# Kernel optimization log

Measured on AMD Instinct MI355X. Metric: run time of the kernel, lower is better.

Reference implementation:

```python
import jax, jax.numpy as jnp
import numpy as np

N_HEAD = 16

def _alibi_slopes(num_heads):
    # m_i = (256 ** (1/num_heads)) ** -(i+1)
    x = (2.0 ** 8) ** (1.0 / num_heads)
    return jnp.asarray([1.0 / x ** (i + 1) for i in range(num_heads)], dtype=jnp.float32)

def setup_inputs() -> dict:
    key = jax.random.key(0)
    k1, k2 = jax.random.split(key)
    B, S, D = 2, 2048, 1024
    x = jax.random.normal(k1, (B, S, D), dtype=jnp.float32)
    W_kqv = jax.random.normal(k2, (D, 3 * D), dtype=jnp.float32) * 0.02
    return {"x": x, "W_kqv": W_kqv}

def reference(x, W_kqv):
    B, S, D = x.shape
    H = N_HEAD
    hd = D // H
    scale = jnp.sqrt(jnp.asarray(D, dtype=x.dtype))  # NOTE: sqrt(n_embd), per source
    kqv = x @ W_kqv                                   # [B,S,3D]
    k, q, v = jnp.split(kqv, 3, axis=-1)              # chunk order: key, query, value
    q = q.reshape(B, S, H, hd).transpose(0, 2, 1, 3)  # [B,H,S,hd]
    k = k.reshape(B, S, H, hd).transpose(0, 2, 1, 3)
    v = v.reshape(B, S, H, hd).transpose(0, 2, 1, 3)
    # ALiBi bias: m[h] * (j - i)
    pos = jnp.arange(S)
    rel = (pos[None, :] - pos[:, None]).astype(x.dtype)      # [S,S]
    m = _alibi_slopes(H).astype(x.dtype)                     # [H]
    bias = m[:, None, None] * rel                            # [H,S,S]
    score = jnp.einsum('bhqd,bhkd->bhqk', q, k) / scale + bias[None]
    causal = pos[None, :] <= pos[:, None]                    # [S,S] lower-tri
    score = jnp.where(causal[None, None], score, -jnp.inf)
    attn = jax.nn.softmax(score, axis=-1)                    # [B,H,S,S]
    out = jnp.einsum('bhqk,bhkd->bhqd', attn, v)
    out = out.transpose(0, 2, 1, 3).reshape(B, S, D)
    return (out, attn)
```

## Files before the change

### kernel.cpp

```cpp
#include <hip/hip_runtime.h>
#include <hip/hip_bf16.h>

typedef __attribute__((ext_vector_type(8))) short short8;
typedef __attribute__((ext_vector_type(4))) float f32x4;

static __device__ __forceinline__ unsigned short f2bf(float f) {
    unsigned int x = __float_as_uint(f);
    x += 0x7fffu + ((x >> 16) & 1u);
    return (unsigned short)(x >> 16);
}

static __device__ __forceinline__ void gld_lds16(const unsigned short* g, unsigned short* l) {
    __builtin_amdgcn_global_load_lds((const __attribute__((address_space(1))) void*)g,
                                     (__attribute__((address_space(3))) void*)l, 16, 0, 0);
}

__global__ __launch_bounds__(256) void cvt_x_kernel(const float* __restrict__ in,
                                                    unsigned short* __restrict__ outb,
                                                    int n4) {
    int i = blockIdx.x * 256 + threadIdx.x;
    if (i < n4) {
        f32x4 v = *(const f32x4*)(in + (size_t)i * 4);
        ushort4 o;
        o.x = f2bf(v[0]); o.y = f2bf(v[1]); o.z = f2bf(v[2]); o.w = f2bf(v[3]);
        *(ushort4*)(outb + (size_t)i * 4) = o;
    }
}

__global__ __launch_bounds__(256) void cvt_wt_kernel(const float* __restrict__ W,
                                                     unsigned short* __restrict__ WT) {
    __shared__ float t[64][65];
    const int n0 = blockIdx.x * 64;
    const int k0 = blockIdx.y * 64;
    const int tid = threadIdx.x;
#pragma unroll
    for (int i = 0; i < 16; ++i) {
        int lin = tid + i * 256;
        int rr = lin >> 6, cc = lin & 63;
        t[rr][cc] = W[(size_t)(k0 + rr) * 3072 + n0 + cc];
    }
    __syncthreads();
#pragma unroll
    for (int i = 0; i < 16; ++i) {
        int lin = tid + i * 256;
        int nn = lin >> 6, kk = lin & 63;
        WT[(size_t)(n0 + nn) * 1024 + k0 + kk] = f2bf(t[kk][nn]);
    }
}

__global__ __launch_bounds__(256) void gemm_kqv_kernel(
    const unsigned short* __restrict__ A,
    const unsigned short* __restrict__ BT,
    unsigned short* __restrict__ qb,
    unsigned short* __restrict__ kb,
    unsigned short* __restrict__ vtb) {
    __shared__ __attribute__((aligned(16))) unsigned short smem[2 * 128 * 72];
    unsigned short (*As)[64] = (unsigned short(*)[64])smem;
    unsigned short (*Bs)[64] = (unsigned short(*)[64])(smem + 128 * 64);
    const int tid = threadIdx.x;
    const int w = tid >> 6, lane = tid & 63;
    const int quad = lane >> 4, cl = lane & 15;

    const int wg = (int)blockIdx.x + 24 * (int)blockIdx.y;
    const int wgs = (wg & 7) * 96 + (wg >> 3);
    const int m0 = (wgs / 24) * 128, n0 = (wgs % 24) * 128;
    const int wm = (w >> 1) * 64, wn = (w & 1) * 64;

    const int srow = lane >> 3;
    const int schk = (lane & 7) ^ srow;
    const unsigned short* Ap = A + (size_t)(m0 + w * 32 + srow) * 1024 + schk * 8;
    const unsigned short* Bp = BT + (size_t)(n0 + w * 32 + srow) * 1024 + schk * 8;

    f32x4 acc[4][4] = {};

    for (int kk = 0; kk < 1024; kk += 64) {
#pragma unroll
        for (int i = 0; i < 4; ++i) {
            gld_lds16(Ap + kk + (size_t)i * 8 * 1024, &As[w * 32 + i * 8][0]);
            gld_lds16(Bp + kk + (size_t)i * 8 * 1024, &Bs[w * 32 + i * 8][0]);
        }
        __syncthreads();
#pragma unroll
        for (int kc = 0; kc < 2; ++kc) {
            short8 af[4], bfr[4];
#pragma unroll
            for (int i = 0; i < 4; ++i) {
                const int col = ((kc * 4 + quad) ^ (cl & 7)) * 8;
                af[i] = *(const short8*)&As[wm + i * 16 + cl][col];
                bfr[i] = *(const short8*)&Bs[wn + i * 16 + cl][col];
            }
#pragma unroll
            for (int im = 0; im < 4; ++im)
#pragma unroll
                for (int in = 0; in < 4; ++in)
                    acc[im][in] = __builtin_amdgcn_mfma_f32_16x16x32_bf16(
                        af[im], bfr[in], acc[im][in], 0, 0, 0);
        }
        __syncthreads();
    }
    unsigned short (*Cs)[130] = (unsigned short(*)[130])smem;

    const int chunk = n0 >> 10;
    const int d0 = n0 & 1023;
    const int b = m0 >> 11;
    const int s_base = m0 & 2047;

    if (chunk == 2) {
#pragma unroll
        for (int im = 0; im < 4; ++im)
#pragma unroll
            for (int in = 0; in < 4; ++in)
#pragma unroll
                for (int rg = 0; rg < 4; ++rg)
                    Cs[wn + in * 16 + cl][wm + im * 16 + quad * 4 + rg] =
                        f2bf(acc[im][in][rg]);
        __syncthreads();
#pragma unroll
        for (int it = 0; it < 8; ++it) {
            int l = it * 2048 + tid * 8;
            int c = l >> 7;
            int r = l & 127;
            int d = d0 + c, hh = d >> 6, dd = d & 63;
            size_t dst = ((size_t)(b * 16 + hh) * 64 + dd) * 2048 + s_base + r;
            *(uint4*)(vtb + dst) = *(const uint4*)&Cs[c][r];
        }
    } else {
#pragma unroll
        for (int im = 0; im < 4; ++im)
#pragma unroll
            for (int in = 0; in < 4; ++in)
#pragma unroll
                for (int rg = 0; rg < 4; ++rg)
                    Cs[wm + im * 16 + quad * 4 + rg][wn + in * 16 + cl] =
                        f2bf(acc[im][in][rg]);
        __syncthreads();
        unsigned short* outp = (chunk == 0) ? kb : qb;
#pragma unroll
        for (int it = 0; it < 8; ++it) {
            int l = it * 2048 + tid * 8;
            int r = l >> 7;
            int c = l & 127;
            int d = d0 + c, hh = d >> 6, dd = d & 63;
            size_t dst = ((size_t)(b * 16 + hh) * 2048 + s_base + r) * 64 + dd;
            *(uint4*)(outp + dst) = *(const uint4*)&Cs[r][c];
        }
    }
}

__global__ __launch_bounds__(256, 2) void attn_kernel(
    const unsigned short* __restrict__ qb,
    const unsigned short* __restrict__ kb,
    const unsigned short* __restrict__ vtb,
    float* __restrict__ out_,
    float* __restrict__ attn) {
    const int h = blockIdx.y;
    const int b = blockIdx.z;
    const int bh = b * 16 + h;
    const int tid = threadIdx.x;
    const int w = tid >> 6;
    const int lane = tid & 63;
    const int quad = lane >> 4;
    const int cl = lane & 15;

    const unsigned short* Qh = qb + (size_t)bh * 2048 * 64;
    const unsigned short* Kh = kb + (size_t)bh * 2048 * 64;
    const unsigned short* Vh = vtb + (size_t)bh * 64 * 2048;
    float* attnh = attn + (size_t)bh * 2048 * 2048;

    __shared__ __attribute__((aligned(16))) unsigned short Kt[2][64][64];
    __shared__ __attribute__((aligned(16))) unsigned short Vt[2][64][64];
    __shared__ __attribute__((aligned(16))) unsigned short Ps[4][16][64];

    const int srow = lane >> 3;
    const int schk = (lane & 7) ^ srow;

    auto stageK = [&](int jt, int buf) {
#pragma unroll
        for (int i = 0; i < 2; ++i)
            gld_lds16(Kh + (size_t)(jt * 64 + w * 16 + i * 8 + srow) * 64 + schk * 8,
                      &Kt[buf][w * 16 + i * 8][0]);
    };
    auto stageV = [&](int j0, int buf) {
#pragma unroll
        for (int i = 0; i < 2; ++i)
            gld_lds16(Vh + (size_t)(w * 16 + i * 8 + srow) * 2048 + j0 + schk * 8,
                      &Vt[buf][w * 16 + i * 8][0]);
    };

    const float mh = exp2f(-0.5f * (float)(h + 1));
    const float sc1 = 1.0f / 32.0f;

    for (int half = 0; half < 2; ++half) {
        const int t64 = half ? 31 - (int)blockIdx.x : (int)blockIdx.x;
        const int q0 = t64 * 64;
        const int row0 = q0 + w * 16;
        const int jtmax = t64;

        short8 aq0 = *(const short8*)(Qh + (size_t)(row0 + cl) * 64 + quad * 8);
        short8 aq1 = *(const short8*)(Qh + (size_t)(row0 + cl) * 64 + 32 + quad * 8);

        float rsum[4] = {0.f, 0.f, 0.f, 0.f};
        __syncthreads();
        stageK(0, 0);
        {
            int cur = 0;
            for (int jt = 0; jt <= jtmax; ++jt, cur ^= 1) {
                __syncthreads();
                if (jt < jtmax) stageK(jt + 1, cur ^ 1);
                const int j0 = jt * 64;
#pragma unroll
                for (int nt = 0; nt < 4; ++nt) {
                    const int r = nt * 16 + cl;
                    short8 k0 = *(const short8*)&Kt[cur][r][((quad) ^ (cl & 7)) * 8];
                    short8 k1 = *(const short8*)&Kt[cur][r][((quad + 4) ^ (cl & 7)) * 8];
                    f32x4 s = {0.f, 0.f, 0.f, 0.f};
                    s = __builtin_amdgcn_mfma_f32_16x16x32_bf16(aq0, k0, s, 0, 0, 0);
                    s = __builtin_amdgcn_mfma_f32_16x16x32_bf16(aq1, k1, s, 0, 0, 0);
                    const int jc = j0 + nt * 16 + cl;
#pragma unroll
                    for (int rg = 0; rg < 4; ++rg) {
                        int irow = row0 + quad * 4 + rg;
                        if (jc <= irow)
                            rsum[rg] += __expf(s[rg] * sc1 + mh * (float)(jc - irow));
                    }
                }
            }
        }
#pragma unroll
        for (int rg = 0; rg < 4; ++rg) {
            float v = rsum[rg];
            v += __shfl_xor(v, 1);
            v += __shfl_xor(v, 2);
            v += __shfl_xor(v, 4);
            v += __shfl_xor(v, 8);
            rsum[rg] = 1.0f / v;
        }

        __syncthreads();
        f32x4 oacc[4] = {};
        stageK(0, 0);
        stageV(0, 0);
        {
            int cur = 0;
            for (int jt = 0; jt <= jtmax; ++jt, cur ^= 1) {
                __syncthreads();
                if (jt < jtmax) {
                    stageK(jt + 1, cur ^ 1);
                    stageV(jt * 64 + 64, cur ^ 1);
                }
                const int j0 = jt * 64;
                f32x4 sv[4];
#pragma unroll
                for (int nt = 0; nt < 4; ++nt) {
                    const int r = nt * 16 + cl;
                    short8 k0 = *(const short8*)&Kt[cur][r][((quad) ^ (cl & 7)) * 8];
                    short8 k1 = *(const short8*)&Kt[cur][r][((quad + 4) ^ (cl & 7)) * 8];
                    f32x4 s = {0.f, 0.f, 0.f, 0.f};
                    s = __builtin_amdgcn_mfma_f32_16x16x32_bf16(aq0, k0, s, 0, 0, 0);
                    sv[nt] = __builtin_amdgcn_mfma_f32_16x16x32_bf16(aq1, k1, s, 0, 0, 0);
                }
#pragma unroll
                for (int nt = 0; nt < 4; ++nt) {
                    const int jc = j0 + nt * 16 + cl;
#pragma unroll
                    for (int rg = 0; rg < 4; ++rg) {
                        const int irow = row0 + quad * 4 + rg;
                        float p = (jc <= irow)
                                      ? __expf(sv[nt][rg] * sc1 + mh * (float)(jc - irow)) * rsum[rg]
                                      : 0.f;
                        Ps[w][quad * 4 + rg]
                          [(((nt * 2 + (cl >> 3)) ^ ((quad * 4 + rg) & 7)) << 3) | (cl & 7)] =
                            f2bf(p);
                        __builtin_nontemporal_store(p, attnh + (size_t)irow * 2048 + jc);
                    }
                }

                short8 pa0 = *(const short8*)&Ps[w][cl][((quad ^ (cl & 7)) << 3)];
                short8 pa1 = *(const short8*)&Ps[w][cl][((((quad + 4)) ^ (cl & 7)) << 3)];

#pragma unroll
                for (int on = 0; on < 4; ++on) {
                    const int r = on * 16 + cl;
                    short8 v0 = *(const short8*)&Vt[cur][r][((quad) ^ (cl & 7)) * 8];
                    short8 v1 = *(const short8*)&Vt[cur][r][((quad + 4) ^ (cl & 7)) * 8];
                    oacc[on] = __builtin_amdgcn_mfma_f32_16x16x32_bf16(pa0, v0, oacc[on], 0, 0, 0);
                    oacc[on] = __builtin_amdgcn_mfma_f32_16x16x32_bf16(pa1, v1, oacc[on], 0, 0, 0);
                }
            }
        }

#pragma unroll
        for (int on = 0; on < 4; ++on) {
#pragma unroll
            for (int rg = 0; rg < 4; ++rg) {
                int srow2 = row0 + quad * 4 + rg;
                __builtin_nontemporal_store(
                    oacc[on][rg], out_ + ((size_t)b * 2048 + srow2) * 1024 + h * 64 + on * 16 + cl);
            }
        }

        const int jz = (jtmax + 1) * 64;
        if (jz < 2048) {
            f32x4 z = {0.f, 0.f, 0.f, 0.f};
            for (int rr = 0; rr < 16; ++rr) {
                float* dst = attnh + (size_t)(row0 + rr) * 2048;
                for (int c = jz + lane * 4; c < 2048; c += 256)
                    __builtin_nontemporal_store(z, (f32x4*)(dst + c));
            }
        }
    }
}

extern "C" void kernel_launch(void* const* d_in, const int* in_sizes, int n_in,
                              void* d_out, int out_size, void* d_ws, size_t ws_size,
                              hipStream_t stream) {
    const float* x = (const float*)d_in[0];
    const float* Wk = (const float*)d_in[1];
    float* out = (float*)d_out;
    float* attn = out + (size_t)2 * 2048 * 1024;

    unsigned short* xb = (unsigned short*)d_ws;
    unsigned short* wtb = xb + (size_t)4096 * 1024;
    unsigned short* qb = wtb + (size_t)3072 * 1024;
    unsigned short* kb = qb + (size_t)32 * 2048 * 64;
    unsigned short* vtb = kb + (size_t)32 * 2048 * 64;

    cvt_x_kernel<<<dim3(4096), dim3(256), 0, stream>>>(x, xb, 4096 * 1024 / 4);
    cvt_wt_kernel<<<dim3(48, 16), dim3(256), 0, stream>>>(Wk, wtb);
    gemm_kqv_kernel<<<dim3(24, 32), dim3(256), 0, stream>>>(xb, wtb, qb, kb, vtb);
    attn_kernel<<<dim3(16, 16, 2), dim3(256), 0, stream>>>(qb, kb, vtb, out, attn);
}
```

Before: 692.4 us.

## Restructure QKV GEMM to 256x256 tiles with double-buffered LDS prefetch

The projection GEMM moves from 128x128 tiles with 4 waves to 256x256 tiles with 8 waves. It double-buffers the LDS tiles so the next K-slice is loaded while MFMAs run, and raises wave priority around the MFMA blocks. The V-transpose epilogue gets an XOR-swizzled LDS staging layout, and the K/Q epilogue now writes scalar bf16 stores directly instead of staging through LDS. The grid shrinks to 192 blocks on a 256-CU part, so fewer CUs are busy, and the direct scalar stores may be less coalesced.

After: 687.0 us. Within noise of the previous version (-0.8%).

```diff
diff --git a/kernel.cpp b/kernel.cpp
--- a/kernel.cpp
+++ b/kernel.cpp
@@ -48,57 +48,83 @@
     }
 }
 
-__global__ __launch_bounds__(256) void gemm_kqv_kernel(
+__global__ __launch_bounds__(512, 2) void gemm_kqv_kernel(
     const unsigned short* __restrict__ A,
     const unsigned short* __restrict__ BT,
     unsigned short* __restrict__ qb,
     unsigned short* __restrict__ kb,
     unsigned short* __restrict__ vtb) {
-    __shared__ __attribute__((aligned(16))) unsigned short smem[2 * 128 * 72];
-    unsigned short (*As)[64] = (unsigned short(*)[64])smem;
-    unsigned short (*Bs)[64] = (unsigned short(*)[64])(smem + 128 * 64);
+    __shared__ __attribute__((aligned(16))) unsigned short smem[2 * 2 * 256 * 64];
+    unsigned short (*As)[256][64] = (unsigned short(*)[256][64])smem;
+    unsigned short (*Bs)[256][64] = (unsigned short(*)[256][64])(smem + 2 * 256 * 64);
     const int tid = threadIdx.x;
     const int w = tid >> 6, lane = tid & 63;
     const int quad = lane >> 4, cl = lane & 15;
 
-    const int wg = (int)blockIdx.x + 24 * (int)blockIdx.y;
-    const int wgs = (wg & 7) * 96 + (wg >> 3);
-    const int m0 = (wgs / 24) * 128, n0 = (wgs % 24) * 128;
-    const int wm = (w >> 1) * 64, wn = (w & 1) * 64;
+    const int wg = (int)blockIdx.x + 12 * (int)blockIdx.y;
+    const int wgs = (wg & 7) * 24 + (wg >> 3);
+    const int m0 = (wgs / 12) * 256, n0 = (wgs % 12) * 256;
+    const int wm = (w >> 2) * 128, wn = (w & 3) * 64;
 
     const int srow = lane >> 3;
     const int schk = (lane & 7) ^ srow;
-    const unsigned short* Ap = A + (size_t)(m0 + w * 32 + srow) * 1024 + schk * 8;
-    const unsigned short* Bp = BT + (size_t)(n0 + w * 32 + srow) * 1024 + schk * 8;
-
-    f32x4 acc[4][4] = {};
-
-    for (int kk = 0; kk < 1024; kk += 64) {
-#pragma unroll
-        for (int i = 0; i < 4; ++i) {
-            gld_lds16(Ap + kk + (size_t)i * 8 * 1024, &As[w * 32 + i * 8][0]);
-            gld_lds16(Bp + kk + (size_t)i * 8 * 1024, &Bs[w * 32 + i * 8][0]);
-        }
-        __syncthreads();
-#pragma unroll
-        for (int kc = 0; kc < 2; ++kc) {
-            short8 af[4], bfr[4];
-#pragma unroll
-            for (int i = 0; i < 4; ++i) {
-                const int col = ((kc * 4 + quad) ^ (cl & 7)) * 8;
-                af[i] = *(const short8*)&As[wm + i * 16 + cl][col];
-                bfr[i] = *(const short8*)&Bs[wn + i * 16 + cl][col];
-            }
-#pragma unroll
-            for (int im = 0; im < 4; ++im)
-#pragma unroll
-                for (int in = 0; in < 4; ++in)
-                    acc[im][in] = __builtin_amdgcn_mfma_f32_16x16x32_bf16(
-                        af[im], bfr[in], acc[im][in], 0, 0, 0);
-        }
-        __syncthreads();
-    }
-    unsigned short (*Cs)[130] = (unsigned short(*)[130])smem;
+    const unsigned short* Ap = A + (size_t)(m0 + w * 8 + srow) * 1024 + schk * 8;
+    const unsigned short* Bp = BT + (size_t)(n0 + w * 8 + srow) * 1024 + schk * 8;
+
+    f32x4 acc[8][4] = {};
+
+    auto stageA = [&](int kk, int buf) {
+#pragma unroll
+        for (int i = 0; i < 4; ++i)
+            gld_lds16(Ap + kk + (size_t)i * 64 * 1024, &As[buf][i * 64 + w * 8][0]);
+    };
+    auto stageB = [&](int kk, int buf) {
+#pragma unroll
+        for (int i = 0; i < 4; ++i)
+            gld_lds16(Bp + kk + (size_t)i * 64 * 1024, &Bs[buf][i * 64 + w * 8][0]);
+    };
+
+    stageA(0, 0);
+    stageB(0, 0);
+
+    for (int kt = 0; kt < 16; ++kt) {
+        const int cur = kt & 1;
+        asm volatile("s_waitcnt vmcnt(0)" ::: "memory");
+        __builtin_amdgcn_s_barrier();
+
+        short8 bfr[4][2];
+#pragma unroll
+        for (int n = 0; n < 4; ++n)
+#pragma unroll
+            for (int kc = 0; kc < 2; ++kc)
+                bfr[n][kc] = *(const short8*)
+                    &Bs[cur][wn + n * 16 + cl][((kc * 4 + quad) ^ (cl & 7)) * 8];
+
+#pragma unroll
+        for (int q = 0; q < 4; ++q) {
+            if (q == 0 && kt < 15) stageA(kt * 64 + 64, cur ^ 1);
+            if (q == 1 && kt < 15) stageB(kt * 64 + 64, cur ^ 1);
+            short8 af[2][2];
+#pragma unroll
+            for (int i = 0; i < 2; ++i)
+#pragma unroll
+                for (int kc = 0; kc < 2; ++kc)
+                    af[i][kc] = *(const short8*)
+                        &As[cur][wm + q * 32 + i * 16 + cl][((kc * 4 + quad) ^ (cl & 7)) * 8];
+            __builtin_amdgcn_s_setprio(1);
+#pragma unroll
+            for (int i = 0; i < 2; ++i)
+#pragma unroll
+                for (int n = 0; n < 4; ++n)
+#pragma unroll
+                    for (int kc = 0; kc < 2; ++kc)
+                        acc[q * 2 + i][n] = __builtin_amdgcn_mfma_f32_16x16x32_bf16(
+                            af[i][kc], bfr[n][kc], acc[q * 2 + i][n], 0, 0, 0);
+            __builtin_amdgcn_s_setprio(0);
+            __builtin_amdgcn_sched_barrier(0);
+            __builtin_amdgcn_s_barrier();
+        }
+    }
 
     const int chunk = n0 >> 10;
     const int d0 = n0 & 1023;
@@ -106,44 +132,43 @@
     const int s_base = m0 & 2047;
 
     if (chunk == 2) {
-#pragma unroll
-        for (int im = 0; im < 4; ++im)
+        unsigned short (*Cs)[256] = (unsigned short(*)[256])smem;
+        __syncthreads();
+#pragma unroll
+        for (int im = 0; im < 8; ++im)
 #pragma unroll
             for (int in = 0; in < 4; ++in)
 #pragma unroll
-                for (int rg = 0; rg < 4; ++rg)
-                    Cs[wn + in * 16 + cl][wm + im * 16 + quad * 4 + rg] =
+                for (int rg = 0; rg < 4; ++rg) {
+                    int dl = wn + in * 16 + cl;
+                    int s = wm + im * 16 + quad * 4 + rg;
+                    Cs[dl][(((s >> 3) ^ (dl & 7)) << 3) | (s & 7)] =
                         f2bf(acc[im][in][rg]);
+                }
         __syncthreads();
 #pragma unroll
-        for (int it = 0; it < 8; ++it) {
-            int l = it * 2048 + tid * 8;
-            int c = l >> 7;
-            int r = l & 127;
-            int d = d0 + c, hh = d >> 6, dd = d & 63;
+        for (int it = 0; it < 16; ++it) {
+            int l = it * 4096 + tid * 8;
+            int dr = l >> 8;
+            int r = l & 255;
+            int d = d0 + dr, hh = d >> 6, dd = d & 63;
             size_t dst = ((size_t)(b * 16 + hh) * 64 + dd) * 2048 + s_base + r;
-            *(uint4*)(vtb + dst) = *(const uint4*)&Cs[c][r];
+            *(uint4*)(vtb + dst) = *(const uint4*)&Cs[dr][(((r >> 3) ^ (dr & 7)) << 3)];
         }
     } else {
-#pragma unroll
-        for (int im = 0; im < 4; ++im)
+        unsigned short* outp = (chunk == 0) ? kb : qb;
+#pragma unroll
+        for (int im = 0; im < 8; ++im)
 #pragma unroll
             for (int in = 0; in < 4; ++in)
 #pragma unroll
-                for (int rg = 0; rg < 4; ++rg)
-                    Cs[wm + im * 16 + quad * 4 + rg][wn + in * 16 + cl] =
+                for (int rg = 0; rg < 4; ++rg) {
+                    int s = s_base + wm + im * 16 + quad * 4 + rg;
+                    int d = d0 + wn + in * 16 + cl;
+                    int hh = d >> 6, dd = d & 63;
+                    outp[((size_t)(b * 16 + hh) * 2048 + s) * 64 + dd] =
                         f2bf(acc[im][in][rg]);
-        __syncthreads();
-        unsigned short* outp = (chunk == 0) ? kb : qb;
-#pragma unroll
-        for (int it = 0; it < 8; ++it) {
-            int l = it * 2048 + tid * 8;
-            int r = l >> 7;
-            int c = l & 127;
-            int d = d0 + c, hh = d >> 6, dd = d & 63;
-            size_t dst = ((size_t)(b * 16 + hh) * 2048 + s_base + r) * 64 + dd;
-            *(uint4*)(outp + dst) = *(const uint4*)&Cs[r][c];
-        }
+                }
     }
 }
 
@@ -327,6 +352,6 @@
 
     cvt_x_kernel<<<dim3(4096), dim3(256), 0, stream>>>(x, xb, 4096 * 1024 / 4);
     cvt_wt_kernel<<<dim3(48, 16), dim3(256), 0, stream>>>(Wk, wtb);
-    gemm_kqv_kernel<<<dim3(24, 32), dim3(256), 0, stream>>>(xb, wtb, qb, kb, vtb);
+    gemm_kqv_kernel<<<dim3(12, 16), dim3(512), 0, stream>>>(xb, wtb, qb, kb, vtb);
     attn_kernel<<<dim3(16, 16, 2), dim3(256), 0, stream>>>(qb, kb, vtb, out, attn);
 }
```
